# Kernel tuning notes

Measured on AMD Instinct MI355X. Metric: run time of the kernel, lower is better.

Reference implementation:

```python
import jax, jax.numpy as jnp
import numpy as np

ENCODER_DIM, HIDDEN_DIM, ATT_DIM = 2048, 1024, 1024
B, P = 128, 196  # batch, num_pixels


def setup_inputs() -> dict:
    key = jax.random.key(0)
    ks = jax.random.split(key, 8)
    s_e = 1.0 / np.sqrt(ENCODER_DIM)
    s_h = 1.0 / np.sqrt(HIDDEN_DIM)
    s_a = 1.0 / np.sqrt(ATT_DIM)
    return {
        "encoder_out": jax.random.normal(ks[0], (B, P, ENCODER_DIM), jnp.float32),
        "decoder_hidden": jax.random.normal(ks[1], (B, HIDDEN_DIM), jnp.float32),
        # nn.Linear params (weight is [out, in] in torch; store transposed for x @ W)
        "W_enc": jax.random.uniform(ks[2], (ENCODER_DIM, ATT_DIM), jnp.float32, -s_e, s_e),
        "b_enc": jax.random.uniform(ks[3], (ATT_DIM,), jnp.float32, -s_e, s_e),
        "W_dec": jax.random.uniform(ks[4], (HIDDEN_DIM, ATT_DIM), jnp.float32, -s_h, s_h),
        "b_dec": jax.random.uniform(ks[5], (ATT_DIM,), jnp.float32, -s_h, s_h),
        "W_full": jax.random.uniform(ks[6], (ATT_DIM,), jnp.float32, -s_a, s_a),
        "b_full": jax.random.uniform(ks[7], (), jnp.float32, -s_a, s_a),
    }


def reference(encoder_out, decoder_hidden, W_enc, b_enc, W_dec, b_dec, W_full, b_full):
    # att1: [B, P, A]; att2: [B, 1, A]
    att1 = jnp.einsum("bpe,ea->bpa", encoder_out, W_enc) + b_enc
    att2 = decoder_hidden @ W_dec + b_dec
    att = jax.nn.relu(att1 + att2[:, None, :])
    scores = jnp.einsum("bpa,a->bp", att, W_full) + b_full  # [B, P]
    alpha = jax.nn.softmax(scores, axis=1)
    context = jnp.einsum("bpe,bp->be", encoder_out, alpha)  # [B, E]
    return (context, alpha)
```

## Files before the change

kernel.cpp:

```cpp
#include <hip/hip_runtime.h>
#include <hip/hip_bf16.h>


#define B_   128
#define P_   196
#define E_   2048
#define H_   1024
#define A_   1024
#define M_   (B_ * P_)
#define NKSTEP (E_ / 64)

typedef __bf16 bf16x8 __attribute__((ext_vector_type(8)));
typedef float f32x4 __attribute__((ext_vector_type(4)));

__device__ __bf16 g_wt[(size_t)A_ * E_];

__device__ __forceinline__ bf16x8 cvt8r(const float4 a, const float4 b) {
    bf16x8 r;
    r[0] = (__bf16)a.x; r[1] = (__bf16)a.y; r[2] = (__bf16)a.z; r[3] = (__bf16)a.w;
    r[4] = (__bf16)b.x; r[5] = (__bf16)b.y; r[6] = (__bf16)b.z; r[7] = (__bf16)b.w;
    return r;
}

__device__ __forceinline__ void gl16(const void* g, void* l) {
    __builtin_amdgcn_global_load_lds(
        (const __attribute__((address_space(1))) unsigned int*)g,
        (__attribute__((address_space(3))) unsigned int*)l, 16, 0, 0);
}

__global__ __launch_bounds__(256) void k_wt(const float* __restrict__ w) {
    __shared__ __bf16 tile[64][72];
    const int t = threadIdx.x;
    const int a0 = blockIdx.x * 64, e0 = blockIdx.y * 64;
    const int er = t >> 2, c0 = (t & 3) * 16;
#pragma unroll
    for (int j = 0; j < 4; ++j) {
        const float4 v =
            *(const float4*)&w[(size_t)(e0 + er) * A_ + a0 + c0 + j * 4];
        tile[c0 + j * 4 + 0][er] = (__bf16)v.x;
        tile[c0 + j * 4 + 1][er] = (__bf16)v.y;
        tile[c0 + j * 4 + 2][er] = (__bf16)v.z;
        tile[c0 + j * 4 + 3][er] = (__bf16)v.w;
    }
    __syncthreads();
    const int ar = t >> 2, es0 = (t & 3) * 16;
    *(bf16x8*)&g_wt[(size_t)(a0 + ar) * E_ + e0 + es0] =
        *(const bf16x8*)&tile[ar][es0];
    *(bf16x8*)&g_wt[(size_t)(a0 + ar) * E_ + e0 + es0 + 8] =
        *(const bf16x8*)&tile[ar][es0 + 8];
}

__global__ __launch_bounds__(256) void k_att2(
    const float* __restrict__ dh, const float* __restrict__ wdec,
    const float* __restrict__ benc, const float* __restrict__ bdec,
    float* __restrict__ scores, float* __restrict__ att2p) {
    const int b = blockIdx.y;
    const int a0 = blockIdx.x * 128;
    const int t = threadIdx.x;
    const int bid = blockIdx.y * 8 + blockIdx.x;
    const int gi = bid * 256 + t;
    if (gi < M_) scores[gi] = 0.f;
    __shared__ float hs[H_];
    __shared__ float red[256];
    for (int i = t; i < H_; i += 256) hs[i] = dh[(size_t)b * H_ + i];
    __syncthreads();
    const int a = a0 + (t & 127);
    const int h0 = (t >> 7) * 512;
    float acc = 0.f;
#pragma unroll 8
    for (int h = 0; h < 512; ++h)
        acc += hs[h0 + h] * wdec[(size_t)(h0 + h) * A_ + a];
    red[t] = acc;
    __syncthreads();
    if (t < 128)
        att2p[(size_t)b * A_ + a0 + t] =
            red[t] + red[t + 128] + benc[a0 + t] + bdec[a0 + t];
}

__global__ __launch_bounds__(256, 2) void k_gemm_scores(
    const float* __restrict__ Am,
    const float* __restrict__ att2p,
    const float* __restrict__ wfull,
    float* __restrict__ scores) {
    __shared__ __align__(16) __bf16 As[2][128 * 72];
    __shared__ __align__(16) __bf16 Bs[2][128 * 64];
    __shared__ float red[2][128];

    const int t = threadIdx.x;
    const int lane = t & 63;
    const int wave = t >> 6;
    const int wm = wave >> 1, wn = wave & 1;
    const int q = lane >> 4, r = lane & 15;
    const int bn = blockIdx.x, bm = blockIdx.y;
    const int m0 = bm * 128, n0 = bn * 128;

    const int srow = t >> 3;
    const int sseg = t & 7;
    const float* aptr = Am + (size_t)(m0 + srow) * E_ + sseg * 8;
    const int bswz = (((t & 7) ^ ((t >> 3) & 7)) << 4);
    const char* wt0 =
        (const char*)g_wt + (size_t)(n0 + srow) * (E_ * 2) + bswz;
    char* bdst0 = (char*)&Bs[0][0] + wave * 1024;
    char* bdst1 = (char*)&Bs[1][0] + wave * 1024;

    f32x4 acc[4][4] = {};
    float4 areg[8];

#pragma unroll
    for (int i = 0; i < 4; ++i) {
        const float* p = aptr + (size_t)(i * 32) * E_;
        areg[2 * i]     = *(const float4*)p;
        areg[2 * i + 1] = *(const float4*)(p + 4);
    }
#pragma unroll
    for (int i = 0; i < 4; ++i)
        gl16(wt0 + (size_t)i * (32 * E_ * 2), bdst0 + i * 4096);
#pragma unroll
    for (int i = 0; i < 4; ++i)
        *(bf16x8*)&As[0][(srow + i * 32) * 72 + sseg * 8] =
            cvt8r(areg[2 * i], areg[2 * i + 1]);

    int cur = 0;
#pragma unroll 2
    for (int kt = 0; kt < NKSTEP; ++kt) {
        asm volatile("s_waitcnt vmcnt(0)" ::: "memory");
        asm volatile("s_waitcnt lgkmcnt(0)" ::: "memory");
        __builtin_amdgcn_s_barrier();

        const __bf16* AsC = &As[cur][0];
        __bf16* AsN = &As[cur ^ 1][0];
        const char* BsC = (const char*)&Bs[cur][0];
        char* bdstN = cur ? bdst0 : bdst1;
        const bool pf = (kt + 1 < NKSTEP);

        if (pf) {
            const float* pa = aptr + (size_t)(kt + 1) * 64;
#pragma unroll
            for (int i = 0; i < 4; ++i) {
                const float* p = pa + (size_t)(i * 32) * E_;
                areg[2 * i]     = *(const float4*)p;
                areg[2 * i + 1] = *(const float4*)(p + 4);
            }
#pragma unroll
            for (int i = 0; i < 4; ++i)
                gl16(wt0 + (size_t)i * (32 * E_ * 2) + (size_t)(kt + 1) * 128,
                     bdstN + i * 4096);
        }

#pragma unroll
        for (int ks = 0; ks < 2; ++ks) {
            bf16x8 af[4], bfv[4];
#pragma unroll
            for (int f = 0; f < 4; ++f)
                af[f] = *(const bf16x8*)&AsC[(wm * 64 + f * 16 + r) * 72 +
                                             ks * 32 + q * 8];
#pragma unroll
            for (int f = 0; f < 4; ++f) {
                const int nf = wn * 64 + f * 16 + r;
                bfv[f] = *(const bf16x8*)(BsC + nf * 128 +
                         ((ks * 64 + q * 16) ^ ((r & 7) << 4)));
            }
#pragma unroll
            for (int fm = 0; fm < 4; ++fm)
#pragma unroll
                for (int fn = 0; fn < 4; ++fn)
                    acc[fm][fn] = __builtin_amdgcn_mfma_f32_16x16x32_bf16(
                        af[fm], bfv[fn], acc[fm][fn], 0, 0, 0);
        }

        if (pf) {
#pragma unroll
            for (int i = 0; i < 4; ++i)
                *(bf16x8*)&AsN[(srow + i * 32) * 72 + sseg * 8] =
                    cvt8r(areg[2 * i], areg[2 * i + 1]);
        }
        cur ^= 1;
    }

    float psum[4][4];
    const float* wfb = wfull + n0 + wn * 64;
#pragma unroll
    for (int fm = 0; fm < 4; ++fm) {
#pragma unroll
        for (int i = 0; i < 4; ++i) {
            const int row_g = m0 + wm * 64 + fm * 16 + q * 4 + i;
            const unsigned bidx = (unsigned)row_g / 196u;
            const float* a2 = att2p + (size_t)bidx * A_ + n0 + wn * 64;
            float s = 0.f;
#pragma unroll
            for (int fn = 0; fn < 4; ++fn) {
                const int cl = fn * 16 + r;
                float v = acc[fm][fn][i] + a2[cl];
                v = fmaxf(v, 0.f);
                s += v * wfb[cl];
            }
            psum[fm][i] = s;
        }
    }
#pragma unroll
    for (int fm = 0; fm < 4; ++fm)
#pragma unroll
        for (int i = 0; i < 4; ++i) {
            float v = psum[fm][i];
            v += __shfl_xor(v, 1);
            v += __shfl_xor(v, 2);
            v += __shfl_xor(v, 4);
            v += __shfl_xor(v, 8);
            if (r == 0) red[wn][wm * 64 + fm * 16 + q * 4 + i] = v;
        }
    __syncthreads();
    if (t < 128) atomicAdd(&scores[m0 + t], red[0][t] + red[1][t]);
}

__global__ __launch_bounds__(256) void k_softmax(
    const float* __restrict__ scores, float* __restrict__ out) {
    const int b = blockIdx.x;
    const int t = threadIdx.x;
    __shared__ float sm[256];
    const bool act = t < P_;
    const float val = act ? scores[b * P_ + t] : 0.f;
    sm[t] = act ? val : -1e30f;
    __syncthreads();
    for (int off = 128; off > 0; off >>= 1) {
        if (t < off) sm[t] = fmaxf(sm[t], sm[t + off]);
        __syncthreads();
    }
    const float mx = sm[0];
    __syncthreads();
    const float e = act ? __expf(val - mx) : 0.f;
    sm[t] = e;
    __syncthreads();
    for (int off = 128; off > 0; off >>= 1) {
        if (t < off) sm[t] = sm[t] + sm[t + off];
        __syncthreads();
    }
    const float inv = 1.0f / sm[0];
    if (act) out[(size_t)B_ * E_ + b * P_ + t] = e * inv;
}

__global__ __launch_bounds__(256) void k_context(
    const float* __restrict__ enc, float* __restrict__ out) {
    const int b = blockIdx.y;
    const int e0 = blockIdx.x * 1024 + threadIdx.x * 4;
    __shared__ float al[P_];
    if (threadIdx.x < P_)
        al[threadIdx.x] = out[(size_t)B_ * E_ + b * P_ + threadIdx.x];
    __syncthreads();
    float ax = 0.f, ay = 0.f, az = 0.f, aw = 0.f;
    const float* base = enc + (size_t)b * P_ * E_ + e0;
#pragma unroll 14
    for (int p = 0; p < P_; ++p) {
        const float4 v = *(const float4*)(base + (size_t)p * E_);
        const float ap = al[p];
        ax += ap * v.x; ay += ap * v.y; az += ap * v.z; aw += ap * v.w;
    }
    float4 sv; sv.x = ax; sv.y = ay; sv.z = az; sv.w = aw;
    *(float4*)(out + (size_t)b * E_ + e0) = sv;
}

extern "C" void kernel_launch(void* const* d_in, const int* in_sizes, int n_in,
                              void* d_out, int out_size, void* d_ws,
                              size_t ws_size, hipStream_t stream) {
    const float* enc   = (const float*)d_in[0];
    const float* dh    = (const float*)d_in[1];
    const float* wenc  = (const float*)d_in[2];
    const float* benc  = (const float*)d_in[3];
    const float* wdec  = (const float*)d_in[4];
    const float* bdec  = (const float*)d_in[5];
    const float* wfull = (const float*)d_in[6];
    float* out = (float*)d_out;

    float* att2p  = out;
    float* scores = (float*)((char*)d_out + 524288);

    k_wt<<<dim3(A_ / 64, E_ / 64), 256, 0, stream>>>(wenc);
    k_att2<<<dim3(8, B_), 256, 0, stream>>>(dh, wdec, benc, bdec, scores,
                                            att2p);
    k_gemm_scores<<<dim3(8, M_ / 128), 256, 0, stream>>>(enc, att2p, wfull,
                                                         scores);
    k_softmax<<<B_, 256, 0, stream>>>(scores, out);
    k_context<<<dim3(2, B_), 256, 0, stream>>>(enc, out);
}
```

Before: 567.1 us.

## Remap GEMM blocks to XCDs and batch decoder projection across eight rows

The scores GEMM now remaps its block index so that blocks landing on the same XCD, assumed to be round-robin by `orig & 7`, get a contiguous range of the linear tile order. Consecutive blocks on one XCD then share the same M row-tile of encoder_out, which should improve reuse of that tile in that XCD's L2. The decoder-hidden projection now computes eight batch rows per block, so each W_dec element is loaded once for eight outputs. That cuts the grid from 1024 to 128 blocks, trading lower parallelism for less redundant weight traffic in a small kernel.

```diff
diff --git a/kernel.cpp b/kernel.cpp
--- a/kernel.cpp
+++ b/kernel.cpp
@@ -54,27 +54,36 @@
     const float* __restrict__ dh, const float* __restrict__ wdec,
     const float* __restrict__ benc, const float* __restrict__ bdec,
     float* __restrict__ scores, float* __restrict__ att2p) {
-    const int b = blockIdx.y;
+    const int t = threadIdx.x;
     const int a0 = blockIdx.x * 128;
-    const int t = threadIdx.x;
+    const int b0 = blockIdx.y * 8;
     const int bid = blockIdx.y * 8 + blockIdx.x;
     const int gi = bid * 256 + t;
     if (gi < M_) scores[gi] = 0.f;
-    __shared__ float hs[H_];
-    __shared__ float red[256];
-    for (int i = t; i < H_; i += 256) hs[i] = dh[(size_t)b * H_ + i];
+    __shared__ float hs[8][H_];
+    __shared__ float red[256][8];
+    for (int i = t; i < 8 * H_; i += 256)
+        hs[i >> 10][i & 1023] = dh[(size_t)(b0 + (i >> 10)) * H_ + (i & 1023)];
     __syncthreads();
     const int a = a0 + (t & 127);
     const int h0 = (t >> 7) * 512;
-    float acc = 0.f;
-#pragma unroll 8
-    for (int h = 0; h < 512; ++h)
-        acc += hs[h0 + h] * wdec[(size_t)(h0 + h) * A_ + a];
-    red[t] = acc;
-    __syncthreads();
-    if (t < 128)
-        att2p[(size_t)b * A_ + a0 + t] =
-            red[t] + red[t + 128] + benc[a0 + t] + bdec[a0 + t];
+    float acc[8] = {};
+#pragma unroll 4
+    for (int h = 0; h < 512; ++h) {
+        const float w = wdec[(size_t)(h0 + h) * A_ + a];
+#pragma unroll
+        for (int j = 0; j < 8; ++j) acc[j] += hs[j][h0 + h] * w;
+    }
+#pragma unroll
+    for (int j = 0; j < 8; ++j) red[t][j] = acc[j];
+    __syncthreads();
+    if (t < 128) {
+        const float bb = benc[a0 + t] + bdec[a0 + t];
+#pragma unroll
+        for (int j = 0; j < 8; ++j)
+            att2p[(size_t)(b0 + j) * A_ + a0 + t] =
+                red[t][j] + red[t + 128][j] + bb;
+    }
 }
 
 __global__ __launch_bounds__(256, 2) void k_gemm_scores(
@@ -91,7 +100,9 @@
     const int wave = t >> 6;
     const int wm = wave >> 1, wn = wave & 1;
     const int q = lane >> 4, r = lane & 15;
-    const int bn = blockIdx.x, bm = blockIdx.y;
+    const int orig = blockIdx.y * 8 + blockIdx.x;
+    const int L = (orig & 7) * (M_ / 128) + (orig >> 3);
+    const int bn = L & 7, bm = L >> 3;
     const int m0 = bm * 128, n0 = bn * 128;
 
     const int srow = t >> 3;
@@ -274,7 +285,7 @@
     float* scores = (float*)((char*)d_out + 524288);
 
     k_wt<<<dim3(A_ / 64, E_ / 64), 256, 0, stream>>>(wenc);
-    k_att2<<<dim3(8, B_), 256, 0, stream>>>(dh, wdec, benc, bdec, scores,
+    k_att2<<<dim3(8, 16), 256, 0, stream>>>(dh, wdec, benc, bdec, scores,
                                             att2p);
     k_gemm_scores<<<dim3(8, M_ / 128), 256, 0, stream>>>(enc, att2p, wfull,
                                                          scores);
```

New measurement: 553.7 us. 1.02x faster.
